# Optimization experiments

Measured on AMD Instinct MI355X. Metric: run time of the kernel, lower is better.

The kernel has to match this reference:

```python
import jax, jax.numpy as jnp
import numpy as np

GRID = 16
N = GRID * GRID          # num_nodes = 256
D = 64                   # embed_dim
SPARSITY = 0.8
BATCH = 2048


def setup_inputs() -> dict:
    key = jax.random.key(0)
    ks = jax.random.split(key, 11)
    s1 = 1.0 / np.sqrt(D)          # fan_in of per-node Linears
    s2 = 1.0 / np.sqrt(N * D)      # fan_in of global_pool first Linear
    x = jax.random.normal(ks[0], (BATCH, N * D), dtype=jnp.float32)
    adj_param = jax.random.normal(ks[1], (N, N), dtype=jnp.float32) * 0.1
    W1 = jax.random.uniform(ks[2], (N, D, D), minval=-s1, maxval=s1, dtype=jnp.float32)
    b1 = jax.random.uniform(ks[3], (N, D), minval=-s1, maxval=s1, dtype=jnp.float32)
    W2 = jax.random.uniform(ks[4], (N, D, D), minval=-s1, maxval=s1, dtype=jnp.float32)
    b2 = jax.random.uniform(ks[5], (N, D), minval=-s1, maxval=s1, dtype=jnp.float32)
    gpW1 = jax.random.uniform(ks[6], (N * D, D), minval=-s2, maxval=s2, dtype=jnp.float32)
    gpb1 = jax.random.uniform(ks[7], (D,), minval=-s2, maxval=s2, dtype=jnp.float32)
    gpW2 = jax.random.uniform(ks[8], (D, D // 2), minval=-s1, maxval=s1, dtype=jnp.float32)
    gpb2 = jax.random.uniform(ks[9], (D // 2,), minval=-s1, maxval=s1, dtype=jnp.float32)
    return {"x": x, "adj_param": adj_param, "W1": W1, "b1": b1, "W2": W2, "b2": b2,
            "gpW1": gpW1, "gpb1": gpb1, "gpW2": gpW2, "gpb2": gpb2}


def _adjacency(adj_param):
    adj = jax.nn.sigmoid(adj_param)
    # threshold = sorted(flat adj)[int(sparsity * N*N)], then hard-threshold, then zero diagonal
    thr = jnp.sort(adj.reshape(-1))[int(SPARSITY * N * N)]
    adj = adj * (adj > thr)
    return adj * (1.0 - jnp.eye(N, dtype=adj.dtype))


def reference(x, adj_param, W1, b1, W2, b2, gpW1, gpb1, gpW2, gpb2):
    B = x.shape[0]
    adj = _adjacency(adj_param)
    xn = x.reshape(B, N, D)                                    # [B, N, D]
    # per-node distinct MLP == grouped GEMM with weights [N, D, D]
    h = jax.nn.relu(jnp.einsum('bnd,nde->bne', xn, W1) + b1)   # [B, N, D]
    node = jnp.einsum('bnd,nde->bne', h, W2) + b2              # [B, N, D]
    # adjacency-weighted neighbor sum: mixed[b,i] = sum_j adj[i,j] * node[b,j]
    mixed = jnp.einsum('ij,bjd->bid', adj, node)               # [B, N, D]
    final = 0.5 * mixed + 0.5 * node                           # residual mix
    g = jax.nn.relu(final.reshape(B, N * D) @ gpW1 + gpb1)     # [B, D]
    out = g @ gpW2 + gpb2                                      # [B, D//2]
    return out, adj
```

## Files before the change

### kernel.cpp

```cpp
#include <hip/hip_runtime.h>
#include <math.h>

typedef unsigned int uint;
typedef unsigned short ushort;
typedef short short8 __attribute__((ext_vector_type(8)));
typedef float f32x4 __attribute__((ext_vector_type(4)));

#define B_ 2048
#define N_ 256
#define D_ 64
#define ND_ 16384
#define NN_ 65536
#define KIDX_ 52428u
#define NGROUPS 16

#define WS_W1T    ((size_t)0)
#define WS_W2T    ((size_t)2*1024*1024)
#define WS_EFF    ((size_t)4*1024*1024)
#define WS_ADJT   ((size_t)6*1024*1024)
#define WS_GPARTS ((size_t)8*1024*1024)
#define WS_SCAL   ((size_t)16*1024*1024)

__device__ __forceinline__ ushort f2bf(float f) {
    uint u = __float_as_uint(f);
    u += 0x7fffu + ((u >> 16) & 1u);
    return (ushort)(u >> 16);
}
__device__ __forceinline__ float bf2f(ushort u) { return __uint_as_float(((uint)u) << 16); }

__device__ __forceinline__ float sigmoid_exact(float a) {
    float t = (float)exp(-(double)a);
    return 1.0f / (1.0f + t);
}

__device__ __forceinline__ int wfrag_off(int e, int k) {
    return ((((e >> 4) * 2 + (k >> 5)) * 4 + ((k >> 3) & 3)) * 16 + (e & 15)) * 8 + (k & 7);
}

__device__ __forceinline__ void glds16(const ushort* g, ushort* l) {
    __builtin_amdgcn_global_load_lds(
        (const __attribute__((address_space(1))) ushort*)g,
        (__attribute__((address_space(3))) ushort*)l, 16, 0, 0);
}

__global__ __launch_bounds__(256) void k_convert(const float* __restrict__ W1,
                                                 const float* __restrict__ W2,
                                                 ushort* __restrict__ W1f,
                                                 ushort* __restrict__ W2f) {
    int bid = blockIdx.x, tid = threadIdx.x;
    __shared__ ushort P[4096] __attribute__((aligned(16)));
    const float* src = (bid < 256) ? W1 + (size_t)bid * 4096 : W2 + (size_t)(bid - 256) * 4096;
#pragma unroll
    for (int i = 0; i < 16; i++) {
        int idx = i * 256 + tid;
        int k = idx >> 6, e = idx & 63;
        P[wfrag_off(e, k)] = f2bf(src[idx]);
    }
    __syncthreads();
    ushort* dst = (bid < 256) ? W1f + (size_t)bid * 4096 : W2f + (size_t)(bid - 256) * 4096;
#pragma unroll
    for (int i = 0; i < 2; i++)
        ((uint4*)dst)[i * 256 + tid] = ((const uint4*)P)[i * 256 + tid];
}

__global__ __launch_bounds__(1024, 4) void k_radix_select(const float* __restrict__ adj_param,
                                                          uint* __restrict__ scal) {
    __shared__ uint histL[256 * 64];
    __shared__ uint wsum[4];
    __shared__ uint bc[2];
    int tid = threadIdx.x;
    int lane = tid & 63;
    uint prefix = 0;
    uint rank = KIDX_;
    const uint4* pv = (const uint4*)adj_param;
#pragma unroll 1
    for (int pass = 0; pass < 4; pass++) {
        int shift = 24 - 8 * pass;
        for (int i = tid; i < 256 * 64; i += 1024) histL[i] = 0u;
        __syncthreads();
#pragma unroll 1
        for (int i = 0; i < 16; i++) {
            uint4 b4 = pv[i * 1024 + tid];
#pragma unroll
            for (int c = 0; c < 4; c++) {
                uint bits = (c == 0) ? b4.x : (c == 1) ? b4.y : (c == 2) ? b4.z : b4.w;
                uint key = bits ^ ((bits & 0x80000000u) ? 0xFFFFFFFFu : 0x80000000u);
                bool cand = (pass == 0) || ((key >> (32 - 8 * pass)) == prefix);
                if (cand) atomicAdd(&histL[(((key >> shift) & 0xffu) << 6) + lane], 1u);
            }
        }
        __syncthreads();
        uint s0 = 0, sc = 0;
        if (tid < 256) {
#pragma unroll
            for (int l = 0; l < 64; l++) s0 += histL[(tid << 6) + ((l + tid) & 63)];
            sc = s0;
#pragma unroll
            for (int o = 1; o < 64; o <<= 1) {
                uint t = __shfl_up(sc, o, 64);
                if ((tid & 63) >= o) sc += t;
            }
            if ((tid & 63) == 63) wsum[tid >> 6] = sc;
        }
        __syncthreads();
        if (tid < 256) {
            uint base = 0;
#pragma unroll
            for (int w = 0; w < 4; w++)
                if (w < (tid >> 6)) base += wsum[w];
            uint incl = base + sc;
            uint excl = incl - s0;
            if (excl <= rank && rank < incl) {
                bc[0] = (prefix << 8) | (uint)tid;
                bc[1] = rank - excl;
            }
        }
        __syncthreads();
        prefix = bc[0];
        rank = bc[1];
        __syncthreads();
    }
    if (tid == 0) {
        uint key = prefix;
        uint bits = (key & 0x80000000u) ? (key ^ 0x80000000u) : ~key;
        scal[0] = __float_as_uint(sigmoid_exact(__uint_as_float(bits)));
    }
}

__global__ __launch_bounds__(256) void k_thresh(const float* __restrict__ adj_param,
                                                const uint* __restrict__ scal,
                                                float* __restrict__ adj_out,
                                                ushort* __restrict__ adjTF) {
    int i = blockIdx.x * 256 + threadIdx.x;
    float thr = __uint_as_float(scal[0]);
    float s = sigmoid_exact(adj_param[i]);
    int r = i >> 8, c = i & 255;
    float v = (s > thr && r != c) ? s : 0.0f;
    adj_out[i] = v;
    uint chunk = ((((uint)(c >> 4) * 8u + (uint)(r >> 5)) * 4u + (uint)((r >> 3) & 3)) * 16u + (uint)(c & 15));
    adjTF[chunk * 8u + (uint)(r & 7)] = f2bf(v);
}

__global__ __launch_bounds__(256) void k_eff(const float* __restrict__ gpW1,
                                             const ushort* __restrict__ adjTF,
                                             ushort* __restrict__ effF) {
    __shared__ ushort Bf[16384] __attribute__((aligned(16)));
    int d = blockIdx.x, jt = blockIdx.y, tid = threadIdx.x;
#pragma unroll
    for (int t = 0; t < 16; t++) {
        int idx = t * 256 + tid;
        int i = idx >> 4;
        int f4 = idx & 15;
        float4 v = *(const float4*)(gpW1 + ((size_t)i * 64 + d) * 64 + f4 * 4);
        int slab = i >> 6, il = i & 63, e0 = f4 * 4;
        Bf[slab * 4096 + wfrag_off(e0 + 0, il)] = f2bf(v.x);
        Bf[slab * 4096 + wfrag_off(e0 + 1, il)] = f2bf(v.y);
        Bf[slab * 4096 + wfrag_off(e0 + 2, il)] = f2bf(v.z);
        Bf[slab * 4096 + wfrag_off(e0 + 3, il)] = f2bf(v.w);
    }
    __syncthreads();
    int wid = tid >> 6, lane = tid & 63, quad = lane >> 4, l16 = lane & 15;
    f32x4 acc[4];
#pragma unroll
    for (int nt = 0; nt < 4; nt++) acc[nt] = (f32x4){0.f, 0.f, 0.f, 0.f};
#pragma unroll
    for (int ks8 = 0; ks8 < 8; ks8++) {
        short8 af = *(const short8*)&adjTF[(size_t)(((((jt * 4 + wid) * 8 + ks8) * 4 + quad) * 16 + l16)) * 8];
        int slab = ks8 >> 1, ks = ks8 & 1;
#pragma unroll
        for (int nt = 0; nt < 4; nt++) {
            short8 bf = *(const short8*)&Bf[slab * 4096 + (((nt * 2 + ks) * 4 + quad) * 16 + l16) * 8];
            acc[nt] = __builtin_amdgcn_mfma_f32_16x16x32_bf16(af, bf, acc[nt], 0, 0, 0);
        }
    }
#pragma unroll
    for (int nt = 0; nt < 4; nt++) {
        int e = nt * 16 + l16;
#pragma unroll
        for (int r = 0; r < 4; r++) {
            int j = jt * 64 + wid * 16 + quad * 4 + r;
            float w = gpW1[((size_t)j * 64 + d) * 64 + e];
            float eff = 0.5f * (acc[nt][r] + w);
            effF[(size_t)j * 4096 + wfrag_off(e, d)] = f2bf(eff);
        }
    }
}

__global__ __launch_bounds__(256, 2) void k_fused(const float* __restrict__ x,
                                                  const ushort* __restrict__ W1f,
                                                  const ushort* __restrict__ W2f,
                                                  const ushort* __restrict__ effF,
                                                  const float* __restrict__ b1,
                                                  const float* __restrict__ b2,
                                                  float* __restrict__ gparts) {
    __shared__ ushort Wf1[2][4096] __attribute__((aligned(16)));
    __shared__ ushort Wf2[2][4096] __attribute__((aligned(16)));
    __shared__ ushort Ef[2][4096] __attribute__((aligned(16)));
    __shared__ ushort St[4][16 * 72];
    __shared__ float Bs[2][16][64];
    int tid = threadIdx.x;
    int g = blockIdx.x, bt = blockIdx.y;
    int wid = tid >> 6, lane = tid & 63, quad = lane >> 4, l16 = lane & 15;
    int rbase = bt * 64 + wid * 16;
    ushort* Sw = &St[wid][0];

    {
        const float* b1g = b1 + (size_t)g * 1024;
        const float* b2g = b2 + (size_t)g * 1024;
#pragma unroll
        for (int i = 0; i < 4; i++) {
            ((float*)Bs[0])[i * 256 + tid] = b1g[i * 256 + tid];
            ((float*)Bs[1])[i * 256 + tid] = b2g[i * 256 + tid];
        }
    }

    const float* xrow = x + (size_t)(rbase + l16) * ND_ + quad * 8;

    {
        int n0 = g * 16;
        int wo = wid * 1024;
#pragma unroll
        for (int i = 0; i < 2; i++) {
            int off = wo + i * 512;
            glds16(W1f + (size_t)n0 * 4096 + off + lane * 8, &Wf1[0][off]);
            glds16(W2f + (size_t)n0 * 4096 + off + lane * 8, &Wf2[0][off]);
            glds16(effF + (size_t)n0 * 4096 + off + lane * 8, &Ef[0][off]);
        }
    }
    float4 xr0, xr1, xr2, xr3;
    {
        const float* xp = xrow + (size_t)(g * 16) * 64;
        xr0 = *(const float4*)(xp);
        xr1 = *(const float4*)(xp + 4);
        xr2 = *(const float4*)(xp + 32);
        xr3 = *(const float4*)(xp + 36);
    }

    f32x4 accg[4];
#pragma unroll
    for (int nt = 0; nt < 4; nt++) accg[nt] = (f32x4){0.f, 0.f, 0.f, 0.f};

    __syncthreads();

#pragma unroll 1
    for (int nl = 0; nl < 16; nl++) {
        int cur = nl & 1;

        short8 fa0, fa1;
        {
            short8 a;
            a[0] = (short)f2bf(xr0.x); a[1] = (short)f2bf(xr0.y);
            a[2] = (short)f2bf(xr0.z); a[3] = (short)f2bf(xr0.w);
            a[4] = (short)f2bf(xr1.x); a[5] = (short)f2bf(xr1.y);
            a[6] = (short)f2bf(xr1.z); a[7] = (short)f2bf(xr1.w);
            fa0 = a;
            short8 b;
            b[0] = (short)f2bf(xr2.x); b[1] = (short)f2bf(xr2.y);
            b[2] = (short)f2bf(xr2.z); b[3] = (short)f2bf(xr2.w);
            b[4] = (short)f2bf(xr3.x); b[5] = (short)f2bf(xr3.y);
            b[6] = (short)f2bf(xr3.z); b[7] = (short)f2bf(xr3.w);
            fa1 = b;
        }

        if (nl < 15) {
            int nn = g * 16 + nl + 1;
            int wo = wid * 1024;
#pragma unroll
            for (int i = 0; i < 2; i++) {
                int off = wo + i * 512;
                glds16(W1f + (size_t)nn * 4096 + off + lane * 8, &Wf1[cur ^ 1][off]);
                glds16(W2f + (size_t)nn * 4096 + off + lane * 8, &Wf2[cur ^ 1][off]);
                glds16(effF + (size_t)nn * 4096 + off + lane * 8, &Ef[cur ^ 1][off]);
            }
            const float* xp = xrow + (size_t)nn * 64;
            xr0 = *(const float4*)(xp);
            xr1 = *(const float4*)(xp + 4);
            xr2 = *(const float4*)(xp + 32);
            xr3 = *(const float4*)(xp + 36);
        }

        float bias1[4], bias2[4];
#pragma unroll
        for (int nt = 0; nt < 4; nt++) {
            bias1[nt] = Bs[0][nl][nt * 16 + l16];
            bias2[nt] = Bs[1][nl][nt * 16 + l16];
        }

        f32x4 acc[4];
#pragma unroll
        for (int nt = 0; nt < 4; nt++) acc[nt] = (f32x4){0.f, 0.f, 0.f, 0.f};
#pragma unroll
        for (int nt = 0; nt < 4; nt++) {
            short8 bf = *(const short8*)&Wf1[cur][(((nt * 2 + 0) * 4 + quad) * 16 + l16) * 8];
            acc[nt] = __builtin_amdgcn_mfma_f32_16x16x32_bf16(fa0, bf, acc[nt], 0, 0, 0);
        }
#pragma unroll
        for (int nt = 0; nt < 4; nt++) {
            short8 bf = *(const short8*)&Wf1[cur][(((nt * 2 + 1) * 4 + quad) * 16 + l16) * 8];
            acc[nt] = __builtin_amdgcn_mfma_f32_16x16x32_bf16(fa1, bf, acc[nt], 0, 0, 0);
        }
#pragma unroll
        for (int nt = 0; nt < 4; nt++)
#pragma unroll
            for (int r = 0; r < 4; r++) {
                float h = fmaxf(acc[nt][r] + bias1[nt], 0.0f);
                Sw[(quad * 4 + r) * 72 + nt * 16 + l16] = f2bf(h);
            }
        f32x4 acc2[4];
#pragma unroll
        for (int nt = 0; nt < 4; nt++) acc2[nt] = (f32x4){0.f, 0.f, 0.f, 0.f};
#pragma unroll
        for (int ks = 0; ks < 2; ks++) {
            short8 a2 = *(const short8*)&Sw[l16 * 72 + ks * 32 + quad * 8];
#pragma unroll
            for (int nt = 0; nt < 4; nt++) {
                short8 bf = *(const short8*)&Wf2[cur][(((nt * 2 + ks) * 4 + quad) * 16 + l16) * 8];
                acc2[nt] = __builtin_amdgcn_mfma_f32_16x16x32_bf16(a2, bf, acc2[nt], 0, 0, 0);
            }
        }
#pragma unroll
        for (int nt = 0; nt < 4; nt++)
#pragma unroll
            for (int r = 0; r < 4; r++) {
                float v = acc2[nt][r] + bias2[nt];
                Sw[(quad * 4 + r) * 72 + nt * 16 + l16] = f2bf(v);
            }
#pragma unroll
        for (int ks = 0; ks < 2; ks++) {
            short8 a3 = *(const short8*)&Sw[l16 * 72 + ks * 32 + quad * 8];
#pragma unroll
            for (int nt = 0; nt < 4; nt++) {
                short8 bf = *(const short8*)&Ef[cur][(((nt * 2 + ks) * 4 + quad) * 16 + l16) * 8];
                accg[nt] = __builtin_amdgcn_mfma_f32_16x16x32_bf16(a3, bf, accg[nt], 0, 0, 0);
            }
        }

        if (nl < 15) __syncthreads();
    }

    float* gp = gparts + ((size_t)g * B_ + bt * 64) * 64;
#pragma unroll
    for (int nt = 0; nt < 4; nt++)
#pragma unroll
        for (int r = 0; r < 4; r++) {
            int b_loc = wid * 16 + quad * 4 + r;
            int e = nt * 16 + l16;
            gp[b_loc * 64 + e] = accg[nt][r];
        }
}

__global__ __launch_bounds__(64) void k_gp2(const float* __restrict__ gparts,
                                            const float* __restrict__ gpb1,
                                            const float* __restrict__ gpW2,
                                            const float* __restrict__ gpb2,
                                            float* __restrict__ out) {
    __shared__ float gs[64];
    int b = blockIdx.x, e = threadIdx.x;
    float s = gpb1[e];
#pragma unroll
    for (int p = 0; p < NGROUPS; p++) s += gparts[((size_t)p * B_ + b) * 64 + e];
    gs[e] = fmaxf(s, 0.0f);
    __syncthreads();
    if (e < 32) {
        float a = gpb2[e];
#pragma unroll 8
        for (int k2 = 0; k2 < 64; k2++) a += gs[k2] * gpW2[k2 * 32 + e];
        out[(size_t)b * 32 + e] = a;
    }
}

extern "C" void kernel_launch(void* const* d_in, const int* in_sizes, int n_in,
                              void* d_out, int out_size, void* d_ws, size_t ws_size,
                              hipStream_t stream) {
    const float* x = (const float*)d_in[0];
    const float* adj_param = (const float*)d_in[1];
    const float* W1 = (const float*)d_in[2];
    const float* b1 = (const float*)d_in[3];
    const float* W2 = (const float*)d_in[4];
    const float* b2 = (const float*)d_in[5];
    const float* gpW1 = (const float*)d_in[6];
    const float* gpb1 = (const float*)d_in[7];
    const float* gpW2 = (const float*)d_in[8];
    const float* gpb2 = (const float*)d_in[9];

    float* out = (float*)d_out;
    float* adj_out = (float*)d_out + NN_;

    char* ws = (char*)d_ws;
    ushort* W1f = (ushort*)(ws + WS_W1T);
    ushort* W2f = (ushort*)(ws + WS_W2T);
    ushort* effF = (ushort*)(ws + WS_EFF);
    ushort* adjTF = (ushort*)(ws + WS_ADJT);
    float* gparts = (float*)(ws + WS_GPARTS);
    uint* scal = (uint*)(ws + WS_SCAL);

    k_convert<<<512, 256, 0, stream>>>(W1, W2, W1f, W2f);
    k_radix_select<<<1, 1024, 0, stream>>>(adj_param, scal);
    k_thresh<<<256, 256, 0, stream>>>(adj_param, scal, adj_out, adjTF);
    k_eff<<<dim3(64, 4), 256, 0, stream>>>(gpW1, adjTF, effF);
    k_fused<<<dim3(NGROUPS, 32), 256, 0, stream>>>(x, W1f, W2f, effF, b1, b2, gparts);
    k_gp2<<<2048, 64, 0, stream>>>(gparts, gpb1, gpW2, gpb2, out);
}
```

Measured before the change: 278.8 us.

## Fuse six launches into three: merge convert+radix, thresh+eff, and fold final MLP into fused kernel

Merges the weight-conversion and radix-select kernels into one launch, with block 0 running the radix select at 256 threads instead of 1024. The threshold step is folded into the effective-weight kernel, so each block recomputes its adjacency tile in shared memory rather than reading a global bf16 buffer. The final pooled MLP is moved into the tail of the fused kernel, where the last group block per batch tile is chosen through an atomic counter. This removes three launches and a global round trip, at the cost of a slower single-block radix select, repeated sigmoid work across blocks, and a serial tail in the last block.

```diff
diff --git a/kernel.cpp b/kernel.cpp
--- a/kernel.cpp
+++ b/kernel.cpp
@@ -17,9 +17,9 @@
 #define WS_W1T    ((size_t)0)
 #define WS_W2T    ((size_t)2*1024*1024)
 #define WS_EFF    ((size_t)4*1024*1024)
-#define WS_ADJT   ((size_t)6*1024*1024)
 #define WS_GPARTS ((size_t)8*1024*1024)
 #define WS_SCAL   ((size_t)16*1024*1024)
+#define WS_CNT    (WS_SCAL + 256)
 
 __device__ __forceinline__ ushort f2bf(float f) {
     uint u = __float_as_uint(f);
@@ -37,38 +37,48 @@
     return ((((e >> 4) * 2 + (k >> 5)) * 4 + ((k >> 3) & 3)) * 16 + (e & 15)) * 8 + (k & 7);
 }
 
+__device__ __forceinline__ int afrag_off(int jl, int i) {
+    return (((((jl >> 4) * 8 + (i >> 5)) * 4 + ((i >> 3) & 3)) * 16) + (jl & 15)) * 8 + (i & 7);
+}
+
 __device__ __forceinline__ void glds16(const ushort* g, ushort* l) {
     __builtin_amdgcn_global_load_lds(
         (const __attribute__((address_space(1))) ushort*)g,
         (__attribute__((address_space(3))) ushort*)l, 16, 0, 0);
 }
 
-__global__ __launch_bounds__(256) void k_convert(const float* __restrict__ W1,
-                                                 const float* __restrict__ W2,
-                                                 ushort* __restrict__ W1f,
-                                                 ushort* __restrict__ W2f) {
+__global__ __launch_bounds__(256) void k_cvt_radix(const float* __restrict__ W1,
+                                                   const float* __restrict__ W2,
+                                                   const float* __restrict__ adj_param,
+                                                   ushort* __restrict__ W1f,
+                                                   ushort* __restrict__ W2f,
+                                                   uint* __restrict__ scal,
+                                                   uint* __restrict__ cnt) {
+    __shared__ uint SH[16390] __attribute__((aligned(16)));
     int bid = blockIdx.x, tid = threadIdx.x;
-    __shared__ ushort P[4096] __attribute__((aligned(16)));
-    const float* src = (bid < 256) ? W1 + (size_t)bid * 4096 : W2 + (size_t)(bid - 256) * 4096;
-#pragma unroll
-    for (int i = 0; i < 16; i++) {
-        int idx = i * 256 + tid;
-        int k = idx >> 6, e = idx & 63;
-        P[wfrag_off(e, k)] = f2bf(src[idx]);
-    }
-    __syncthreads();
-    ushort* dst = (bid < 256) ? W1f + (size_t)bid * 4096 : W2f + (size_t)(bid - 256) * 4096;
-#pragma unroll
-    for (int i = 0; i < 2; i++)
-        ((uint4*)dst)[i * 256 + tid] = ((const uint4*)P)[i * 256 + tid];
-}
-
-__global__ __launch_bounds__(1024, 4) void k_radix_select(const float* __restrict__ adj_param,
-                                                          uint* __restrict__ scal) {
-    __shared__ uint histL[256 * 64];
-    __shared__ uint wsum[4];
-    __shared__ uint bc[2];
-    int tid = threadIdx.x;
+
+    if (bid != 0) {
+        ushort* P = (ushort*)SH;
+        int b = bid - 1;
+        const float* src = (b < 256) ? W1 + (size_t)b * 4096 : W2 + (size_t)(b - 256) * 4096;
+#pragma unroll
+        for (int i = 0; i < 16; i++) {
+            int idx = i * 256 + tid;
+            int k = idx >> 6, e = idx & 63;
+            P[wfrag_off(e, k)] = f2bf(src[idx]);
+        }
+        __syncthreads();
+        ushort* dst = (b < 256) ? W1f + (size_t)b * 4096 : W2f + (size_t)(b - 256) * 4096;
+#pragma unroll
+        for (int i = 0; i < 2; i++)
+            ((uint4*)dst)[i * 256 + tid] = ((const uint4*)P)[i * 256 + tid];
+        return;
+    }
+
+    if (tid < 32) cnt[tid] = 0u;
+    uint* histL = SH;
+    uint* wsum = SH + 16384;
+    uint* bc = SH + 16388;
     int lane = tid & 63;
     uint prefix = 0;
     uint rank = KIDX_;
@@ -76,22 +86,27 @@
 #pragma unroll 1
     for (int pass = 0; pass < 4; pass++) {
         int shift = 24 - 8 * pass;
-        for (int i = tid; i < 256 * 64; i += 1024) histL[i] = 0u;
-        __syncthreads();
-#pragma unroll 1
-        for (int i = 0; i < 16; i++) {
-            uint4 b4 = pv[i * 1024 + tid];
-#pragma unroll
-            for (int c = 0; c < 4; c++) {
-                uint bits = (c == 0) ? b4.x : (c == 1) ? b4.y : (c == 2) ? b4.z : b4.w;
-                uint key = bits ^ ((bits & 0x80000000u) ? 0xFFFFFFFFu : 0x80000000u);
-                bool cand = (pass == 0) || ((key >> (32 - 8 * pass)) == prefix);
-                if (cand) atomicAdd(&histL[(((key >> shift) & 0xffu) << 6) + lane], 1u);
+        for (int i = tid; i < 256 * 64; i += 256) histL[i] = 0u;
+        __syncthreads();
+#pragma unroll 1
+        for (int ib = 0; ib < 8; ib++) {
+            uint4 v[8];
+#pragma unroll
+            for (int u = 0; u < 8; u++) v[u] = pv[(ib * 8 + u) * 256 + tid];
+#pragma unroll
+            for (int u = 0; u < 8; u++) {
+#pragma unroll
+                for (int c = 0; c < 4; c++) {
+                    uint bits = (c == 0) ? v[u].x : (c == 1) ? v[u].y : (c == 2) ? v[u].z : v[u].w;
+                    uint key = bits ^ ((bits & 0x80000000u) ? 0xFFFFFFFFu : 0x80000000u);
+                    bool cand = (pass == 0) || ((key >> (32 - 8 * pass)) == prefix);
+                    if (cand) atomicAdd(&histL[(((key >> shift) & 0xffu) << 6) + lane], 1u);
+                }
             }
         }
         __syncthreads();
         uint s0 = 0, sc = 0;
-        if (tid < 256) {
+        {
 #pragma unroll
             for (int l = 0; l < 64; l++) s0 += histL[(tid << 6) + ((l + tid) & 63)];
             sc = s0;
@@ -103,7 +118,7 @@
             if ((tid & 63) == 63) wsum[tid >> 6] = sc;
         }
         __syncthreads();
-        if (tid < 256) {
+        {
             uint base = 0;
 #pragma unroll
             for (int w = 0; w < 4; w++)
@@ -127,25 +142,29 @@
     }
 }
 
-__global__ __launch_bounds__(256) void k_thresh(const float* __restrict__ adj_param,
+__global__ __launch_bounds__(256) void k_threff(const float* __restrict__ adj_param,
                                                 const uint* __restrict__ scal,
+                                                const float* __restrict__ gpW1,
                                                 float* __restrict__ adj_out,
-                                                ushort* __restrict__ adjTF) {
-    int i = blockIdx.x * 256 + threadIdx.x;
-    float thr = __uint_as_float(scal[0]);
-    float s = sigmoid_exact(adj_param[i]);
-    int r = i >> 8, c = i & 255;
-    float v = (s > thr && r != c) ? s : 0.0f;
-    adj_out[i] = v;
-    uint chunk = ((((uint)(c >> 4) * 8u + (uint)(r >> 5)) * 4u + (uint)((r >> 3) & 3)) * 16u + (uint)(c & 15));
-    adjTF[chunk * 8u + (uint)(r & 7)] = f2bf(v);
-}
-
-__global__ __launch_bounds__(256) void k_eff(const float* __restrict__ gpW1,
-                                             const ushort* __restrict__ adjTF,
-                                             ushort* __restrict__ effF) {
+                                                ushort* __restrict__ effF) {
+    __shared__ ushort adjS[16384] __attribute__((aligned(16)));
     __shared__ ushort Bf[16384] __attribute__((aligned(16)));
     int d = blockIdx.x, jt = blockIdx.y, tid = threadIdx.x;
+    float thr = __uint_as_float(scal[0]);
+
+    {
+        int jl = tid & 63;
+        int jglob = jt * 64 + jl;
+        int wrow = tid >> 6;
+#pragma unroll 1
+        for (int i = 0; i < 64; i++) {
+            int ir = i * 4 + wrow;
+            float s = sigmoid_exact(adj_param[(size_t)ir * 256 + jglob]);
+            float v = (s > thr && ir != jglob) ? s : 0.0f;
+            adjS[afrag_off(jl, ir)] = f2bf(v);
+            if (d == 0) adj_out[(size_t)ir * 256 + jglob] = v;
+        }
+    }
 #pragma unroll
     for (int t = 0; t < 16; t++) {
         int idx = t * 256 + tid;
@@ -165,7 +184,7 @@
     for (int nt = 0; nt < 4; nt++) acc[nt] = (f32x4){0.f, 0.f, 0.f, 0.f};
 #pragma unroll
     for (int ks8 = 0; ks8 < 8; ks8++) {
-        short8 af = *(const short8*)&adjTF[(size_t)(((((jt * 4 + wid) * 8 + ks8) * 4 + quad) * 16 + l16)) * 8];
+        short8 af = *(const short8*)&adjS[((((wid * 8 + ks8) * 4 + quad) * 16 + l16)) * 8];
         int slab = ks8 >> 1, ks = ks8 & 1;
 #pragma unroll
         for (int nt = 0; nt < 4; nt++) {
@@ -192,12 +211,18 @@
                                                   const ushort* __restrict__ effF,
                                                   const float* __restrict__ b1,
                                                   const float* __restrict__ b2,
-                                                  float* __restrict__ gparts) {
+                                                  float* __restrict__ gparts,
+                                                  const float* __restrict__ gpb1,
+                                                  const float* __restrict__ gpW2,
+                                                  const float* __restrict__ gpb2,
+                                                  float* __restrict__ out,
+                                                  uint* __restrict__ cnt) {
     __shared__ ushort Wf1[2][4096] __attribute__((aligned(16)));
     __shared__ ushort Wf2[2][4096] __attribute__((aligned(16)));
     __shared__ ushort Ef[2][4096] __attribute__((aligned(16)));
     __shared__ ushort St[4][16 * 72];
     __shared__ float Bs[2][16][64];
+    __shared__ int isLast;
     int tid = threadIdx.x;
     int g = blockIdx.x, bt = blockIdx.y;
     int wid = tid >> 6, lane = tid & 63, quad = lane >> 4, l16 = lane & 15;
@@ -347,25 +372,39 @@
             int e = nt * 16 + l16;
             gp[b_loc * 64 + e] = accg[nt][r];
         }
-}
-
-__global__ __launch_bounds__(64) void k_gp2(const float* __restrict__ gparts,
-                                            const float* __restrict__ gpb1,
-                                            const float* __restrict__ gpW2,
-                                            const float* __restrict__ gpb2,
-                                            float* __restrict__ out) {
-    __shared__ float gs[64];
-    int b = blockIdx.x, e = threadIdx.x;
-    float s = gpb1[e];
-#pragma unroll
-    for (int p = 0; p < NGROUPS; p++) s += gparts[((size_t)p * B_ + b) * 64 + e];
-    gs[e] = fmaxf(s, 0.0f);
+
     __syncthreads();
-    if (e < 32) {
-        float a = gpb2[e];
+    if (tid == 0) {
+        __threadfence();
+        isLast = (atomicAdd(&cnt[bt], 1u) == NGROUPS - 1);
+    }
+    __syncthreads();
+    if (!isLast) return;
+    __threadfence();
+
+    float* Gs = (float*)Wf1;
+    float* Wq = (float*)Ef;
+#pragma unroll
+    for (int i = 0; i < 8; i++) Wq[i * 256 + tid] = gpW2[i * 256 + tid];
+#pragma unroll 1
+    for (int i = 0; i < 16; i++) {
+        int lin = i * 256 + tid;
+        int r = lin >> 6, e = lin & 63;
+        float s = gpb1[e];
+#pragma unroll
+        for (int p = 0; p < NGROUPS; p++)
+            s += gparts[((size_t)p * B_ + bt * 64 + r) * 64 + e];
+        Gs[r * 64 + e] = fmaxf(s, 0.0f);
+    }
+    __syncthreads();
+#pragma unroll 1
+    for (int i = 0; i < 8; i++) {
+        int lin = i * 256 + tid;
+        int r = lin >> 5, o = lin & 31;
+        float a = gpb2[o];
 #pragma unroll 8
-        for (int k2 = 0; k2 < 64; k2++) a += gs[k2] * gpW2[k2 * 32 + e];
-        out[(size_t)b * 32 + e] = a;
+        for (int k2 = 0; k2 < 64; k2++) a += Gs[r * 64 + k2] * Wq[k2 * 32 + o];
+        out[(size_t)(bt * 64 + r) * 32 + o] = a;
     }
 }
 
@@ -390,14 +429,12 @@
     ushort* W1f = (ushort*)(ws + WS_W1T);
     ushort* W2f = (ushort*)(ws + WS_W2T);
     ushort* effF = (ushort*)(ws + WS_EFF);
-    ushort* adjTF = (ushort*)(ws + WS_ADJT);
     float* gparts = (float*)(ws + WS_GPARTS);
     uint* scal = (uint*)(ws + WS_SCAL);
-
-    k_convert<<<512, 256, 0, stream>>>(W1, W2, W1f, W2f);
-    k_radix_select<<<1, 1024, 0, stream>>>(adj_param, scal);
-    k_thresh<<<256, 256, 0, stream>>>(adj_param, scal, adj_out, adjTF);
-    k_eff<<<dim3(64, 4), 256, 0, stream>>>(gpW1, adjTF, effF);
-    k_fused<<<dim3(NGROUPS, 32), 256, 0, stream>>>(x, W1f, W2f, effF, b1, b2, gparts);
-    k_gp2<<<2048, 64, 0, stream>>>(gparts, gpb1, gpW2, gpb2, out);
-}
+    uint* cnt = (uint*)(ws + WS_CNT);
+
+    k_cvt_radix<<<513, 256, 0, stream>>>(W1, W2, adj_param, W1f, W2f, scal, cnt);
+    k_threff<<<dim3(64, 4), 256, 0, stream>>>(adj_param, scal, gpW1, adj_out, effF);
+    k_fused<<<dim3(NGROUPS, 32), 256, 0, stream>>>(x, W1f, W2f, effF, b1, b2, gparts,
+                                                   gpb1, gpW2, gpb2, out, cnt);
+}
```

Result: slower. 334.8 us (+20.1%).

## Merge prep kernels and switch fused kernel to register-staged single LDS buffer

Applied to the files above, without the earlier changes.

Weight conversion and the radix-select threshold search now share one launch, with block 0 doing the selection and the other blocks converting weights. Thresholding is folded into the effective-weight kernel, and the intermediate transposed adjacency buffer is dropped, so there are two fewer launches. The fused main kernel drops its double-buffered async global-to-LDS loads and the LDS bias table. It now prefetches the next node's weights and biases into registers, then writes them into a single LDS buffer between two barriers, raising occupancy to 4 blocks per SM. The risks are the extra barrier per node and less load/compute overlap, plus redundant sigmoid work in every k_threff block.

```diff
diff --git a/kernel.cpp b/kernel.cpp
--- a/kernel.cpp
+++ b/kernel.cpp
@@ -17,7 +17,6 @@
 #define WS_W1T    ((size_t)0)
 #define WS_W2T    ((size_t)2*1024*1024)
 #define WS_EFF    ((size_t)4*1024*1024)
-#define WS_ADJT   ((size_t)6*1024*1024)
 #define WS_GPARTS ((size_t)8*1024*1024)
 #define WS_SCAL   ((size_t)16*1024*1024)
 
@@ -37,38 +36,41 @@
     return ((((e >> 4) * 2 + (k >> 5)) * 4 + ((k >> 3) & 3)) * 16 + (e & 15)) * 8 + (k & 7);
 }
 
-__device__ __forceinline__ void glds16(const ushort* g, ushort* l) {
-    __builtin_amdgcn_global_load_lds(
-        (const __attribute__((address_space(1))) ushort*)g,
-        (__attribute__((address_space(3))) ushort*)l, 16, 0, 0);
-}
-
-__global__ __launch_bounds__(256) void k_convert(const float* __restrict__ W1,
-                                                 const float* __restrict__ W2,
-                                                 ushort* __restrict__ W1f,
-                                                 ushort* __restrict__ W2f) {
+__device__ __forceinline__ int afrag_off(int jl, int i) {
+    return (((((jl >> 4) * 8 + (i >> 5)) * 4 + ((i >> 3) & 3)) * 16) + (jl & 15)) * 8 + (i & 7);
+}
+
+__global__ __launch_bounds__(1024) void k_cvt_radix(const float* __restrict__ W1,
+                                                    const float* __restrict__ W2,
+                                                    const float* __restrict__ adj_param,
+                                                    ushort* __restrict__ W1f,
+                                                    ushort* __restrict__ W2f,
+                                                    uint* __restrict__ scal) {
+    __shared__ uint SH[16390] __attribute__((aligned(16)));
     int bid = blockIdx.x, tid = threadIdx.x;
-    __shared__ ushort P[4096] __attribute__((aligned(16)));
-    const float* src = (bid < 256) ? W1 + (size_t)bid * 4096 : W2 + (size_t)(bid - 256) * 4096;
-#pragma unroll
-    for (int i = 0; i < 16; i++) {
-        int idx = i * 256 + tid;
-        int k = idx >> 6, e = idx & 63;
-        P[wfrag_off(e, k)] = f2bf(src[idx]);
-    }
-    __syncthreads();
-    ushort* dst = (bid < 256) ? W1f + (size_t)bid * 4096 : W2f + (size_t)(bid - 256) * 4096;
-#pragma unroll
-    for (int i = 0; i < 2; i++)
-        ((uint4*)dst)[i * 256 + tid] = ((const uint4*)P)[i * 256 + tid];
-}
-
-__global__ __launch_bounds__(1024, 4) void k_radix_select(const float* __restrict__ adj_param,
-                                                          uint* __restrict__ scal) {
-    __shared__ uint histL[256 * 64];
-    __shared__ uint wsum[4];
-    __shared__ uint bc[2];
-    int tid = threadIdx.x;
+
+    if (bid != 0) {
+        int q = tid >> 8, t = tid & 255;
+        int m = (bid - 1) * 4 + q;
+        ushort* P = (ushort*)SH + q * 4096;
+        const float* src = (m < 256) ? W1 + (size_t)m * 4096 : W2 + (size_t)(m - 256) * 4096;
+#pragma unroll
+        for (int i = 0; i < 16; i++) {
+            int idx = i * 256 + t;
+            int k = idx >> 6, e = idx & 63;
+            P[wfrag_off(e, k)] = f2bf(src[idx]);
+        }
+        __syncthreads();
+        ushort* dst = (m < 256) ? W1f + (size_t)m * 4096 : W2f + (size_t)(m - 256) * 4096;
+#pragma unroll
+        for (int i = 0; i < 2; i++)
+            ((uint4*)dst)[i * 256 + t] = ((const uint4*)P)[i * 256 + t];
+        return;
+    }
+
+    uint* histL = SH;
+    uint* wsum = SH + 16384;
+    uint* bc = SH + 16388;
     int lane = tid & 63;
     uint prefix = 0;
     uint rank = KIDX_;
@@ -97,8 +99,8 @@
             sc = s0;
 #pragma unroll
             for (int o = 1; o < 64; o <<= 1) {
-                uint t = __shfl_up(sc, o, 64);
-                if ((tid & 63) >= o) sc += t;
+                uint t2 = __shfl_up(sc, o, 64);
+                if ((tid & 63) >= o) sc += t2;
             }
             if ((tid & 63) == 63) wsum[tid >> 6] = sc;
         }
@@ -127,25 +129,29 @@
     }
 }
 
-__global__ __launch_bounds__(256) void k_thresh(const float* __restrict__ adj_param,
+__global__ __launch_bounds__(256) void k_threff(const float* __restrict__ adj_param,
                                                 const uint* __restrict__ scal,
+                                                const float* __restrict__ gpW1,
                                                 float* __restrict__ adj_out,
-                                                ushort* __restrict__ adjTF) {
-    int i = blockIdx.x * 256 + threadIdx.x;
-    float thr = __uint_as_float(scal[0]);
-    float s = sigmoid_exact(adj_param[i]);
-    int r = i >> 8, c = i & 255;
-    float v = (s > thr && r != c) ? s : 0.0f;
-    adj_out[i] = v;
-    uint chunk = ((((uint)(c >> 4) * 8u + (uint)(r >> 5)) * 4u + (uint)((r >> 3) & 3)) * 16u + (uint)(c & 15));
-    adjTF[chunk * 8u + (uint)(r & 7)] = f2bf(v);
-}
-
-__global__ __launch_bounds__(256) void k_eff(const float* __restrict__ gpW1,
-                                             const ushort* __restrict__ adjTF,
-                                             ushort* __restrict__ effF) {
+                                                ushort* __restrict__ effF) {
+    __shared__ ushort adjS[16384] __attribute__((aligned(16)));
     __shared__ ushort Bf[16384] __attribute__((aligned(16)));
     int d = blockIdx.x, jt = blockIdx.y, tid = threadIdx.x;
+    float thr = __uint_as_float(scal[0]);
+
+    {
+        int jl = tid & 63;
+        int jglob = jt * 64 + jl;
+        int wrow = tid >> 6;
+#pragma unroll 1
+        for (int i = 0; i < 64; i++) {
+            int ir = i * 4 + wrow;
+            float s = sigmoid_exact(adj_param[(size_t)ir * 256 + jglob]);
+            float v = (s > thr && ir != jglob) ? s : 0.0f;
+            adjS[afrag_off(jl, ir)] = f2bf(v);
+            if (d == 0) adj_out[(size_t)ir * 256 + jglob] = v;
+        }
+    }
 #pragma unroll
     for (int t = 0; t < 16; t++) {
         int idx = t * 256 + tid;
@@ -165,7 +171,7 @@
     for (int nt = 0; nt < 4; nt++) acc[nt] = (f32x4){0.f, 0.f, 0.f, 0.f};
 #pragma unroll
     for (int ks8 = 0; ks8 < 8; ks8++) {
-        short8 af = *(const short8*)&adjTF[(size_t)(((((jt * 4 + wid) * 8 + ks8) * 4 + quad) * 16 + l16)) * 8];
+        short8 af = *(const short8*)&adjS[((((wid * 8 + ks8) * 4 + quad) * 16 + l16)) * 8];
         int slab = ks8 >> 1, ks = ks8 & 1;
 #pragma unroll
         for (int nt = 0; nt < 4; nt++) {
@@ -186,55 +192,48 @@
     }
 }
 
-__global__ __launch_bounds__(256, 2) void k_fused(const float* __restrict__ x,
+__global__ __launch_bounds__(256, 4) void k_fused(const float* __restrict__ x,
                                                   const ushort* __restrict__ W1f,
                                                   const ushort* __restrict__ W2f,
                                                   const ushort* __restrict__ effF,
                                                   const float* __restrict__ b1,
                                                   const float* __restrict__ b2,
                                                   float* __restrict__ gparts) {
-    __shared__ ushort Wf1[2][4096] __attribute__((aligned(16)));
-    __shared__ ushort Wf2[2][4096] __attribute__((aligned(16)));
-    __shared__ ushort Ef[2][4096] __attribute__((aligned(16)));
+    __shared__ ushort Wf1[4096] __attribute__((aligned(16)));
+    __shared__ ushort Wf2[4096] __attribute__((aligned(16)));
+    __shared__ ushort Ef[4096] __attribute__((aligned(16)));
     __shared__ ushort St[4][16 * 72];
-    __shared__ float Bs[2][16][64];
     int tid = threadIdx.x;
     int g = blockIdx.x, bt = blockIdx.y;
     int wid = tid >> 6, lane = tid & 63, quad = lane >> 4, l16 = lane & 15;
     int rbase = bt * 64 + wid * 16;
     ushort* Sw = &St[wid][0];
-
-    {
-        const float* b1g = b1 + (size_t)g * 1024;
-        const float* b2g = b2 + (size_t)g * 1024;
-#pragma unroll
-        for (int i = 0; i < 4; i++) {
-            ((float*)Bs[0])[i * 256 + tid] = b1g[i * 256 + tid];
-            ((float*)Bs[1])[i * 256 + tid] = b2g[i * 256 + tid];
-        }
-    }
-
     const float* xrow = x + (size_t)(rbase + l16) * ND_ + quad * 8;
 
-    {
-        int n0 = g * 16;
-        int wo = wid * 1024;
-#pragma unroll
-        for (int i = 0; i < 2; i++) {
-            int off = wo + i * 512;
-            glds16(W1f + (size_t)n0 * 4096 + off + lane * 8, &Wf1[0][off]);
-            glds16(W2f + (size_t)n0 * 4096 + off + lane * 8, &Wf2[0][off]);
-            glds16(effF + (size_t)n0 * 4096 + off + lane * 8, &Ef[0][off]);
-        }
-    }
+    int n0 = g * 16;
+    uint4 w1a = ((const uint4*)(W1f + (size_t)n0 * 4096))[tid];
+    uint4 w1b = ((const uint4*)(W1f + (size_t)n0 * 4096))[256 + tid];
+    uint4 w2a = ((const uint4*)(W2f + (size_t)n0 * 4096))[tid];
+    uint4 w2b = ((const uint4*)(W2f + (size_t)n0 * 4096))[256 + tid];
+    uint4 ea  = ((const uint4*)(effF + (size_t)n0 * 4096))[tid];
+    uint4 eb  = ((const uint4*)(effF + (size_t)n0 * 4096))[256 + tid];
     float4 xr0, xr1, xr2, xr3;
     {
-        const float* xp = xrow + (size_t)(g * 16) * 64;
+        const float* xp = xrow + (size_t)n0 * 64;
         xr0 = *(const float4*)(xp);
         xr1 = *(const float4*)(xp + 4);
         xr2 = *(const float4*)(xp + 32);
         xr3 = *(const float4*)(xp + 36);
     }
+    float b1n[4], b2n[4];
+#pragma unroll
+    for (int nt = 0; nt < 4; nt++) {
+        b1n[nt] = b1[n0 * 64 + nt * 16 + l16];
+        b2n[nt] = b2[n0 * 64 + nt * 16 + l16];
+    }
+    ((uint4*)Wf1)[tid] = w1a;  ((uint4*)Wf1)[256 + tid] = w1b;
+    ((uint4*)Wf2)[tid] = w2a;  ((uint4*)Wf2)[256 + tid] = w2b;
+    ((uint4*)Ef)[tid]  = ea;   ((uint4*)Ef)[256 + tid]  = eb;
 
     f32x4 accg[4];
 #pragma unroll
@@ -244,8 +243,6 @@
 
 #pragma unroll 1
     for (int nl = 0; nl < 16; nl++) {
-        int cur = nl & 1;
-
         short8 fa0, fa1;
         {
             short8 a;
@@ -261,42 +258,41 @@
             b[6] = (short)f2bf(xr3.z); b[7] = (short)f2bf(xr3.w);
             fa1 = b;
         }
+        float bias1[4], bias2[4];
+#pragma unroll
+        for (int nt = 0; nt < 4; nt++) { bias1[nt] = b1n[nt]; bias2[nt] = b2n[nt]; }
 
         if (nl < 15) {
             int nn = g * 16 + nl + 1;
-            int wo = wid * 1024;
-#pragma unroll
-            for (int i = 0; i < 2; i++) {
-                int off = wo + i * 512;
-                glds16(W1f + (size_t)nn * 4096 + off + lane * 8, &Wf1[cur ^ 1][off]);
-                glds16(W2f + (size_t)nn * 4096 + off + lane * 8, &Wf2[cur ^ 1][off]);
-                glds16(effF + (size_t)nn * 4096 + off + lane * 8, &Ef[cur ^ 1][off]);
-            }
+            w1a = ((const uint4*)(W1f + (size_t)nn * 4096))[tid];
+            w1b = ((const uint4*)(W1f + (size_t)nn * 4096))[256 + tid];
+            w2a = ((const uint4*)(W2f + (size_t)nn * 4096))[tid];
+            w2b = ((const uint4*)(W2f + (size_t)nn * 4096))[256 + tid];
+            ea  = ((const uint4*)(effF + (size_t)nn * 4096))[tid];
+            eb  = ((const uint4*)(effF + (size_t)nn * 4096))[256 + tid];
             const float* xp = xrow + (size_t)nn * 64;
             xr0 = *(const float4*)(xp);
             xr1 = *(const float4*)(xp + 4);
             xr2 = *(const float4*)(xp + 32);
             xr3 = *(const float4*)(xp + 36);
-        }
-
-        float bias1[4], bias2[4];
+#pragma unroll
+            for (int nt = 0; nt < 4; nt++) {
+                b1n[nt] = b1[nn * 64 + nt * 16 + l16];
+                b2n[nt] = b2[nn * 64 + nt * 16 + l16];
+            }
+        }
+
+        f32x4 acc[4];
+#pragma unroll
+        for (int nt = 0; nt < 4; nt++) acc[nt] = (f32x4){0.f, 0.f, 0.f, 0.f};
 #pragma unroll
         for (int nt = 0; nt < 4; nt++) {
-            bias1[nt] = Bs[0][nl][nt * 16 + l16];
-            bias2[nt] = Bs[1][nl][nt * 16 + l16];
-        }
-
-        f32x4 acc[4];
-#pragma unroll
-        for (int nt = 0; nt < 4; nt++) acc[nt] = (f32x4){0.f, 0.f, 0.f, 0.f};
+            short8 bf = *(const short8*)&Wf1[(((nt * 2 + 0) * 4 + quad) * 16 + l16) * 8];
+            acc[nt] = __builtin_amdgcn_mfma_f32_16x16x32_bf16(fa0, bf, acc[nt], 0, 0, 0);
+        }
 #pragma unroll
         for (int nt = 0; nt < 4; nt++) {
-            short8 bf = *(const short8*)&Wf1[cur][(((nt * 2 + 0) * 4 + quad) * 16 + l16) * 8];
-            acc[nt] = __builtin_amdgcn_mfma_f32_16x16x32_bf16(fa0, bf, acc[nt], 0, 0, 0);
-        }
-#pragma unroll
-        for (int nt = 0; nt < 4; nt++) {
-            short8 bf = *(const short8*)&Wf1[cur][(((nt * 2 + 1) * 4 + quad) * 16 + l16) * 8];
+            short8 bf = *(const short8*)&Wf1[(((nt * 2 + 1) * 4 + quad) * 16 + l16) * 8];
             acc[nt] = __builtin_amdgcn_mfma_f32_16x16x32_bf16(fa1, bf, acc[nt], 0, 0, 0);
         }
 #pragma unroll
@@ -314,7 +310,7 @@
             short8 a2 = *(const short8*)&Sw[l16 * 72 + ks * 32 + quad * 8];
 #pragma unroll
             for (int nt = 0; nt < 4; nt++) {
-                short8 bf = *(const short8*)&Wf2[cur][(((nt * 2 + ks) * 4 + quad) * 16 + l16) * 8];
+                short8 bf = *(const short8*)&Wf2[(((nt * 2 + ks) * 4 + quad) * 16 + l16) * 8];
                 acc2[nt] = __builtin_amdgcn_mfma_f32_16x16x32_bf16(a2, bf, acc2[nt], 0, 0, 0);
             }
         }
@@ -330,12 +326,18 @@
             short8 a3 = *(const short8*)&Sw[l16 * 72 + ks * 32 + quad * 8];
 #pragma unroll
             for (int nt = 0; nt < 4; nt++) {
-                short8 bf = *(const short8*)&Ef[cur][(((nt * 2 + ks) * 4 + quad) * 16 + l16) * 8];
+                short8 bf = *(const short8*)&Ef[(((nt * 2 + ks) * 4 + quad) * 16 + l16) * 8];
                 accg[nt] = __builtin_amdgcn_mfma_f32_16x16x32_bf16(a3, bf, accg[nt], 0, 0, 0);
             }
         }
 
-        if (nl < 15) __syncthreads();
+        if (nl < 15) {
+            __syncthreads();
+            ((uint4*)Wf1)[tid] = w1a;  ((uint4*)Wf1)[256 + tid] = w1b;
+            ((uint4*)Wf2)[tid] = w2a;  ((uint4*)Wf2)[256 + tid] = w2b;
+            ((uint4*)Ef)[tid]  = ea;   ((uint4*)Ef)[256 + tid]  = eb;
+            __syncthreads();
+        }
     }
 
     float* gp = gparts + ((size_t)g * B_ + bt * 64) * 64;
@@ -390,14 +392,11 @@
     ushort* W1f = (ushort*)(ws + WS_W1T);
     ushort* W2f = (ushort*)(ws + WS_W2T);
     ushort* effF = (ushort*)(ws + WS_EFF);
-    ushort* adjTF = (ushort*)(ws + WS_ADJT);
     float* gparts = (float*)(ws + WS_GPARTS);
     uint* scal = (uint*)(ws + WS_SCAL);
 
-    k_convert<<<512, 256, 0, stream>>>(W1, W2, W1f, W2f);
-    k_radix_select<<<1, 1024, 0, stream>>>(adj_param, scal);
-    k_thresh<<<256, 256, 0, stream>>>(adj_param, scal, adj_out, adjTF);
-    k_eff<<<dim3(64, 4), 256, 0, stream>>>(gpW1, adjTF, effF);
+    k_cvt_radix<<<129, 1024, 0, stream>>>(W1, W2, adj_param, W1f, W2f, scal);
+    k_threff<<<dim3(64, 4), 256, 0, stream>>>(adj_param, scal, gpW1, adj_out, effF);
     k_fused<<<dim3(NGROUPS, 32), 256, 0, stream>>>(x, W1f, W2f, effF, b1, b2, gparts);
     k_gp2<<<2048, 64, 0, stream>>>(gparts, gpb1, gpW2, gpb2, out);
 }
```

Result: slower. 287.0 us (+2.9%).
